# Kernel tuning notes

Hardware: AMD Instinct MI355X
Metric: run time of the kernel (lower is better)

Reference implementation:

```python
import jax, jax.numpy as jnp
import numpy as np

IMG_H, IMG_W = 256, 704  # full image shape (img_metas['img_shape'])
EPS = 1e-5
B, N_CAM, D_REF, C_CH = 1, 6, 1, 256
HF, WF = 32, 88
DD = 64
BEV_H = BEV_W = 128
Q = BEV_H * BEV_W


def inverse_sigmoid(x, eps=1e-5):
    x = jnp.clip(x, 0.0, 1.0)
    return jnp.log(jnp.clip(x, eps) / jnp.clip(1.0 - x, eps))


def grid_sample_2d(feat, grid):
    # feat [N,C,H,W], grid [N,Hg,Wg,2] (x,y in [-1,1]); bilinear, zeros padding, align_corners=False
    Nn, C, H, W = feat.shape
    x = (grid[..., 0] + 1.0) * 0.5 * W - 0.5
    y = (grid[..., 1] + 1.0) * 0.5 * H - 0.5
    x0 = jnp.floor(x)
    y0 = jnp.floor(y)
    wx = x - x0
    wy = y - y0
    x0 = x0.astype(jnp.int32)
    y0 = y0.astype(jnp.int32)

    def gather(ix, iy):
        valid = (ix >= 0) & (ix < W) & (iy >= 0) & (iy < H)
        ixc = jnp.clip(ix, 0, W - 1)
        iyc = jnp.clip(iy, 0, H - 1)
        v = jax.vmap(lambda f, jx, jy: f[:, jy, jx])(feat, ixc, iyc)  # [N,C,Hg,Wg]
        return v * valid[:, None].astype(feat.dtype)

    return (gather(x0, y0) * ((1 - wx) * (1 - wy))[:, None]
            + gather(x0 + 1, y0) * (wx * (1 - wy))[:, None]
            + gather(x0, y0 + 1) * ((1 - wx) * wy)[:, None]
            + gather(x0 + 1, y0 + 1) * (wx * wy)[:, None])


def grid_sample_3d(vol, grid):
    # vol [N,C,D,H,W], grid [N,Dg,Hg,Wg,3] (x,y,z); trilinear, zeros padding, align_corners=False
    Nn, C, D, H, W = vol.shape
    x = (grid[..., 0] + 1.0) * 0.5 * W - 0.5
    y = (grid[..., 1] + 1.0) * 0.5 * H - 0.5
    z = (grid[..., 2] + 1.0) * 0.5 * D - 0.5
    x0 = jnp.floor(x); y0 = jnp.floor(y); z0 = jnp.floor(z)
    wx = x - x0; wy = y - y0; wz = z - z0
    x0 = x0.astype(jnp.int32); y0 = y0.astype(jnp.int32); z0 = z0.astype(jnp.int32)

    def gather(ix, iy, iz):
        valid = (ix >= 0) & (ix < W) & (iy >= 0) & (iy < H) & (iz >= 0) & (iz < D)
        ixc = jnp.clip(ix, 0, W - 1)
        iyc = jnp.clip(iy, 0, H - 1)
        izc = jnp.clip(iz, 0, D - 1)
        v = jax.vmap(lambda f, jx, jy, jz: f[:, jz, jy, jx])(vol, ixc, iyc, izc)
        return v * valid[:, None].astype(vol.dtype)

    return (gather(x0, y0, z0) * ((1 - wx) * (1 - wy) * (1 - wz))[:, None]
            + gather(x0 + 1, y0, z0) * (wx * (1 - wy) * (1 - wz))[:, None]
            + gather(x0, y0 + 1, z0) * ((1 - wx) * wy * (1 - wz))[:, None]
            + gather(x0 + 1, y0 + 1, z0) * (wx * wy * (1 - wz))[:, None]
            + gather(x0, y0, z0 + 1) * ((1 - wx) * (1 - wy) * wz)[:, None]
            + gather(x0 + 1, y0, z0 + 1) * (wx * (1 - wy) * wz)[:, None]
            + gather(x0, y0 + 1, z0 + 1) * ((1 - wx) * wy * wz)[:, None]
            + gather(x0 + 1, y0 + 1, z0 + 1) * (wx * wy * wz)[:, None])


def setup_inputs() -> dict:
    key = jax.random.key(0)
    ks = jax.random.split(key, 12)
    feat = jax.random.normal(ks[0], (B * N_CAM, C_CH, HF, WF), jnp.float32)
    bev_queries = jax.random.normal(ks[1], (B, Q, C_CH), jnp.float32)
    bev_pos = jax.random.normal(ks[2], (B, Q, C_CH), jnp.float32)
    reference_points = jax.random.uniform(ks[3], (B, D_REF, Q, 3), jnp.float32)
    pc_range = jnp.array([-51.2, -51.2, -5.0, 51.2, 51.2, 3.0], jnp.float32)
    # semi-realistic lidar->image projection matrices: intrinsics * axis-swap * yaw per camera
    f, cx, cy = 500.0, IMG_W / 2.0, IMG_H / 2.0
    K = np.array([[f, 0, cx, 0], [0, f, cy, 0], [0, 0, 1, 0], [0, 0, 0, 1]], np.float32)
    A = np.array([[0, -1, 0, 0], [0, 0, -1, 0], [1, 0, 0, 0], [0, 0, 0, 1]], np.float32)
    mats = []
    for i in range(N_CAM):
        th = 2.0 * np.pi * i / N_CAM
        c, s = np.cos(th), np.sin(th)
        R = np.array([[c, s, 0, 0], [-s, c, 0, 0], [0, 0, 1, 0], [0, 0, 0, 1]], np.float32)
        mats.append(K @ A @ R)
    lidar_to_img = jnp.asarray(np.stack(mats))[None]  # [1,N,4,4]
    depth_prob = jax.random.uniform(ks[4], (B * N_CAM, DD, HF, WF), jnp.float32)
    sc = 0.02
    return {
        'feat': feat, 'bev_queries': bev_queries, 'bev_pos': bev_pos,
        'reference_points': reference_points, 'pc_range': pc_range,
        'lidar_to_img': lidar_to_img, 'depth_prob': depth_prob,
        'w_pos': jax.random.normal(ks[5], (C_CH, 1), jnp.float32) * sc,
        'b_pos': jnp.zeros((1,), jnp.float32),
        'w_img': jax.random.normal(ks[6], (C_CH, N_CAM * 2), jnp.float32) * sc,
        'b_img': jnp.zeros((N_CAM * 2,), jnp.float32),
        'w_att': jax.random.normal(ks[7], (C_CH, N_CAM), jnp.float32) * sc,
        'b_att': jnp.zeros((N_CAM,), jnp.float32),
        'conv_w': jax.random.normal(ks[8], (C_CH, C_CH, 3, 3), jnp.float32) * sc,
        'conv_b': jnp.zeros((C_CH,), jnp.float32),
        'bn_gamma': jnp.ones((C_CH,), jnp.float32),
        'bn_beta': jnp.zeros((C_CH,), jnp.float32),
        'bn_mean': jnp.zeros((C_CH,), jnp.float32),
        'bn_var': jnp.ones((C_CH,), jnp.float32),
        'se_w': jax.random.normal(ks[9], (C_CH, C_CH), jnp.float32) * sc,
        'se_b': jnp.zeros((C_CH,), jnp.float32),
        'cbam_w': jax.random.normal(ks[10], (1, 2, 7, 7), jnp.float32) * 0.05,
        'cbam_b': jnp.zeros((1,), jnp.float32),
        'bev_h': BEV_H, 'bev_w': BEV_W,
    }


def reference(feat, bev_queries, bev_pos, reference_points, pc_range, lidar_to_img, depth_prob,
              w_pos, b_pos, w_img, b_img, w_att, b_att, conv_w, conv_b,
              bn_gamma, bn_beta, bn_mean, bn_var, se_w, se_b, cbam_w, cbam_b, bev_h, bev_w):
    Bq, Qn = bev_queries.shape[:2]
    D = reference_points.shape[1]
    N = lidar_to_img.shape[1]
    BN, C, Hf, Wf = feat.shape
    q = bev_queries + bev_pos
    pos_offset = q @ w_pos + b_pos  # [B,Q,1] (only_use_height)
    z = jax.nn.sigmoid(inverse_sigmoid(reference_points[..., 2:3]) + pos_offset[:, None])
    rp = jnp.concatenate([reference_points[..., :2], z], axis=-1)  # [B,D,Q,3]
    attn = (q @ w_att + b_att).reshape(Bq, 1, Qn, N, 1)
    img_off = q @ w_img + b_img  # [B,Q,2N]
    # unnormalize to lidar coords; apply_3d_transformation == identity (no aug)
    pts = rp * (pc_range[3:] - pc_range[:3]) + pc_range[:3]
    pts4 = jnp.concatenate([pts, jnp.ones_like(pts[..., :1])], axis=-1)  # [B,D,Q,4]
    cam = jnp.einsum('bnij,bdqj->dbnqi', lidar_to_img, pts4)  # [D,B,N,Q,4]
    ref_depth = cam[..., 2:3]
    mask = ref_depth > EPS
    xy = cam[..., :2] / jnp.maximum(cam[..., 2:3], EPS)
    xy = xy / jnp.array([IMG_W, IMG_H], dtype=xy.dtype)
    xy = (xy - 0.5) * 2.0
    mask = mask & (xy[..., 0:1] > -1.0) & (xy[..., 0:1] < 1.0) & (xy[..., 1:2] > -1.0) & (xy[..., 1:2] < 1.0)
    Dd = depth_prob.shape[1]
    ref_depth = (ref_depth / Dd - 0.5) * 2.0
    mask = mask & (ref_depth > -1.0) & (ref_depth < 1.0)
    bev_mask = jnp.transpose(mask, (1, 4, 3, 2, 0)).astype(feat.dtype)  # [B,1,Q,N,D]
    off = img_off.reshape(Bq, Qn, N, 2).transpose(0, 2, 1, 3)[None] / jnp.array([Wf, Hf], dtype=feat.dtype)
    xy = xy + off  # [D,B,N,Q,2]
    grid = xy.transpose(1, 2, 3, 0, 4).reshape(BN, Qn, D, 2)
    sampled = grid_sample_2d(feat, grid).reshape(Bq, N, C, Qn, D).transpose(0, 2, 3, 1, 4)  # [B,C,Q,N,D]
    grid3 = jnp.concatenate([xy, ref_depth], axis=-1).transpose(1, 2, 3, 0, 4).reshape(BN, 1, Qn, D, 3)
    dp = grid_sample_3d(depth_prob[:, None], grid3).reshape(Bq, N, 1, Qn, D).transpose(0, 2, 3, 1, 4)
    bev_mask = jnp.nan_to_num(dp) * bev_mask
    w = jax.nn.sigmoid(attn) * jnp.nan_to_num(bev_mask)
    agg = (jnp.nan_to_num(sampled) * w)[..., 0].sum(-1)  # [B,C,Q] (D==1)
    x = agg.reshape(Bq, C, bev_h, bev_w)
    dn = ('NCHW', 'OIHW', 'NCHW')
    x = jax.lax.conv_general_dilated(x, conv_w, (1, 1), ((1, 1), (1, 1)), dimension_numbers=dn) + conv_b[None, :, None, None]
    x = (x - bn_mean[None, :, None, None]) * (bn_gamma / jnp.sqrt(bn_var + 1e-5))[None, :, None, None] + bn_beta[None, :, None, None]
    x = jax.nn.relu(x)
    s = x.mean(axis=(2, 3))  # SE: global avg pool + 1x1 conv + sigmoid
    x = x * jax.nn.sigmoid(s @ se_w.T + se_b)[:, :, None, None]
    a = jnp.concatenate([x.max(axis=1, keepdims=True), x.mean(axis=1, keepdims=True)], axis=1)  # CBAM spatial
    a = jax.lax.conv_general_dilated(a, cbam_w, (1, 1), ((3, 3), (3, 3)), dimension_numbers=dn) + cbam_b[None, :, None, None]
    x = x * jax.nn.sigmoid(a)
    out = x.reshape(Bq, C, bev_h * bev_w).transpose(0, 2, 1)
    return out, rp
```

## Files before the change

### kernel.cpp

```cpp
#include <hip/hip_runtime.h>
#include <math.h>

#define QN   16384
#define CCH  256
#define NCAM 6
#define HFD  32
#define WFD  88
#define DDD  64
#define BEVH 128
#define BEVW 128
#define IMGW 704.0f
#define IMGH 256.0f
#define EPSV 1e-5f

typedef __attribute__((ext_vector_type(8))) short bf8_t;
typedef __attribute__((ext_vector_type(8))) unsigned short us8;
typedef __attribute__((ext_vector_type(4))) unsigned short us4;
typedef __attribute__((ext_vector_type(4))) float f4_t;

__device__ __forceinline__ float sigmoidf_(float x){ return 1.0f/(1.0f+__expf(-x)); }

__device__ __forceinline__ unsigned short f2bf(float f){
    unsigned int b = __float_as_uint(f);
    b += 0x7FFFu + ((b >> 16) & 1u);
    return (unsigned short)(b >> 16);
}
__device__ __forceinline__ float bf2f(unsigned short u){
    return __uint_as_float(((unsigned int)u) << 16);
}

__global__ __launch_bounds__(256) void k_prep(const float* __restrict__ feat, unsigned short* __restrict__ feat_tH,
                                              const float* __restrict__ cw, unsigned short* __restrict__ wtH,
                                              float* __restrict__ ssum){
    int b = blockIdx.x;
    if (b < 4224){
        __shared__ float tile[32][33];
        int n   = b / 704;
        int rem = b - n*704;
        int cb  = (rem / 88) * 32;
        int pb  = (rem % 88) * 32;
        int tx = threadIdx.x & 31, ty = threadIdx.x >> 5;
        for (int r = ty; r < 32; r += 8)
            tile[r][tx] = feat[(size_t)(n*256 + cb + r)*2816 + pb + tx];
        __syncthreads();
        for (int r = ty; r < 32; r += 8)
            feat_tH[(size_t)(n*2816 + pb + r)*256 + cb + tx] = f2bf(tile[tx][r]);
    } else {
        int b2 = b - 4224;
        if (b2 == 0) ssum[threadIdx.x] = 0.f;
        int idx = b2*256 + threadIdx.x;
        int ci = idx & 255;
        int co = (idx >> 8) & 255;
        int kk = idx >> 16;
        wtH[idx] = f2bf(cw[(size_t)(co*256 + ci)*9 + kk]);
    }
}

__global__ __launch_bounds__(256) void k_geomagg(
    const float* __restrict__ bq, const float* __restrict__ bpos,
    const float* __restrict__ refp, const float* __restrict__ pcr,
    const float* __restrict__ l2i, const float* __restrict__ dpr,
    const float* __restrict__ w_pos, const float* __restrict__ b_pos,
    const float* __restrict__ w_img, const float* __restrict__ b_img,
    const float* __restrict__ w_att, const float* __restrict__ b_att,
    const unsigned short* __restrict__ feat_tH,
    unsigned short* __restrict__ aggH, float* __restrict__ out_rp)
{
    __shared__ float wl[19][256];
    __shared__ int   so_l[192];
    __shared__ float sw_l[192];
    int q0 = blockIdx.x * 8;
    int tid = threadIdx.x;
    int wid = tid >> 6, lane = tid & 63;
    int c0 = lane * 4;

    wl[0][tid] = w_pos[tid];
    #pragma unroll
    for (int r = 0; r < 6; r++){
        int idx = r*256 + tid;
        int c = idx / 6, j = idx - 6*c;
        wl[1 + j][c] = w_att[idx];
    }
    #pragma unroll
    for (int r = 0; r < 12; r++){
        int idx = r*256 + tid;
        int c = idx / 12, j = idx - 12*c;
        wl[7 + j][c] = w_img[idx];
    }
    __syncthreads();

    #pragma unroll
    for (int qi = 0; qi < 2; qi++){
        int ql = wid*2 + qi;
        int q  = q0 + ql;

        const float4 a4 = *(const float4*)(bq  + (size_t)q*CCH + c0);
        const float4 b4 = *(const float4*)(bpos+ (size_t)q*CCH + c0);
        float qv[4] = {a4.x+b4.x, a4.y+b4.y, a4.z+b4.z, a4.w+b4.w};

        float s[19];
        #pragma unroll
        for (int j = 0; j < 19; j++){
            const float4 wv = *(const float4*)&wl[j][c0];
            s[j] = qv[0]*wv.x + qv[1]*wv.y + qv[2]*wv.z + qv[3]*wv.w;
        }
        #pragma unroll
        for (int off=1; off<64; off<<=1){
            #pragma unroll
            for (int i=0;i<19;i++) s[i] += __shfl_xor(s[i], off, 64);
        }

        float pos_off = s[0] + b_pos[0];
        float rx = refp[q*3+0], ry = refp[q*3+1], rz = refp[q*3+2];
        float zc_ = fminf(fmaxf(rz, 0.f), 1.f);
        float inv = logf(fmaxf(zc_, EPSV) / fmaxf(1.f - zc_, EPSV));
        float znew = sigmoidf_(inv + pos_off);

        if (lane == 0){
            out_rp[q*3+0] = rx; out_rp[q*3+1] = ry; out_rp[q*3+2] = znew;
        }
        if (lane < NCAM){
            int n = lane;
            float att  = s[1+n] + b_att[n];
            float offx = (s[7+2*n]   + b_img[2*n])   / (float)WFD;
            float offy = (s[7+2*n+1] + b_img[2*n+1]) / (float)HFD;
            float lo0=pcr[0], lo1=pcr[1], lo2=pcr[2];
            float hi0=pcr[3], hi1=pcr[4], hi2=pcr[5];
            float px = rx*(hi0-lo0)+lo0, py = ry*(hi1-lo1)+lo1, pz = znew*(hi2-lo2)+lo2;
            const float* M = l2i + n*16;
            float cx = M[0]*px + M[1]*py + M[2]*pz  + M[3];
            float cy = M[4]*px + M[5]*py + M[6]*pz  + M[7];
            float cz = M[8]*px + M[9]*py + M[10]*pz + M[11];
            bool m = cz > EPSV;
            float zdiv = fmaxf(cz, EPSV);
            float u = (cx/zdiv)/IMGW; u = (u - 0.5f)*2.f;
            float v = (cy/zdiv)/IMGH; v = (v - 0.5f)*2.f;
            m = m && (u > -1.f) && (u < 1.f) && (v > -1.f) && (v < 1.f);
            float rdn = (cz/(float)DDD - 0.5f)*2.f;
            m = m && (rdn > -1.f) && (rdn < 1.f);

            int base = ql*24 + n*4;
            float wq = 0.f, xs = 0.f, ys = 0.f;
            if (m){
                float u2 = u + offx, v2 = v + offy;
                xs = (u2 + 1.f)*0.5f*WFD - 0.5f;
                ys = (v2 + 1.f)*0.5f*HFD - 0.5f;
                float zs = (rdn + 1.f)*0.5f*DDD - 0.5f;
                float fx = floorf(xs), fy = floorf(ys), fz = floorf(zs);
                int x0=(int)fx, y0=(int)fy, z0=(int)fz;
                float wx = xs-fx, wy = ys-fy, wz = zs-fz;
                float dp = 0.f;
                const float* vol = dpr + (size_t)n*DDD*HFD*WFD;
                #pragma unroll
                for (int dz=0; dz<2; dz++)
                #pragma unroll
                for (int dy=0; dy<2; dy++)
                #pragma unroll
                for (int dx=0; dx<2; dx++){
                    int ix=x0+dx, iy=y0+dy, iz=z0+dz;
                    if (ix>=0 && ix<WFD && iy>=0 && iy<HFD && iz>=0 && iz<DDD){
                        float ww = (dx?wx:1.f-wx)*(dy?wy:1.f-wy)*(dz?wz:1.f-wz);
                        dp += ww * vol[(size_t)(iz*HFD+iy)*WFD + ix];
                    }
                }
                wq = sigmoidf_(att) * dp;
            }
            if (m && wq != 0.f){
                float fx = floorf(xs), fy = floorf(ys);
                int x0=(int)fx, y0=(int)fy;
                float wx = xs-fx, wy = ys-fy;
                float cwv[4] = {(1.f-wx)*(1.f-wy), wx*(1.f-wy), (1.f-wx)*wy, wx*wy};
                int xi[4] = {x0, x0+1, x0, x0+1};
                int yi[4] = {y0, y0, y0+1, y0+1};
                #pragma unroll
                for (int k=0;k<4;k++){
                    bool ok = (xi[k]>=0 && xi[k]<WFD && yi[k]>=0 && yi[k]<HFD);
                    so_l[base+k] = ok ? ((n*HFD + yi[k])*WFD + xi[k]) : 0;
                    sw_l[base+k] = ok ? wq*cwv[k] : 0.f;
                }
            } else {
                #pragma unroll
                for (int k=0;k<4;k++){ so_l[base+k] = 0; sw_l[base+k] = 0.f; }
            }
        }
    }
    __syncthreads();

    int c4 = lane * 4;
    #pragma unroll
    for (int qi=0; qi<2; qi++){
        int ql = wid*2 + qi;
        float a0=0.f, a1=0.f, a2=0.f, a3=0.f;
        #pragma unroll
        for (int k=0;k<24;k++){
            float w = sw_l[ql*24+k];
            if (w != 0.f){
                us4 v = *(const us4*)(feat_tH + (size_t)so_l[ql*24+k]*CCH + c4);
                a0 += w * bf2f(v.x);
                a1 += w * bf2f(v.y);
                a2 += w * bf2f(v.z);
                a3 += w * bf2f(v.w);
            }
        }
        us4 o; o.x = f2bf(a0); o.y = f2bf(a1); o.z = f2bf(a2); o.w = f2bf(a3);
        *(us4*)(aggH + (size_t)(q0+ql)*CCH + c4) = o;
    }
}

__global__ __launch_bounds__(512, 4) void k_conv2(const unsigned short* __restrict__ aggH,
    const unsigned short* __restrict__ wtH, const float* __restrict__ conv_b,
    const float* __restrict__ bn_g, const float* __restrict__ bn_b,
    const float* __restrict__ bn_m, const float* __restrict__ bn_v,
    float* __restrict__ xN, float* __restrict__ ssum)
{
    __shared__ unsigned short Al[130][72];
    __shared__ unsigned short Bl[3][64][72];
    __shared__ float sacc[64];

    int h   = blockIdx.x;
    int co0 = blockIdx.y * 64;
    int tid  = threadIdx.x;
    int lane = tid & 63, wid = tid >> 6;
    int m_wave = (wid & 3) * 32;
    int n_wave = (wid >> 2) * 32;
    int l15 = lane & 15, quad = lane >> 4;

    f4_t acc[2][2];
    #pragma unroll
    for (int i=0;i<2;i++)
    #pragma unroll
    for (int j=0;j<2;j++) acc[i][j] = (f4_t){0.f,0.f,0.f,0.f};

    int aw = tid >> 2;
    int sa = (tid & 3) * 16;
    int bco = tid >> 3;
    int sb  = (tid & 7) * 8;

    if (tid < 8){
        int r = (tid >> 2) ? 129 : 0;
        int sg = (tid & 3) * 16;
        us8 z = (us8){0,0,0,0,0,0,0,0};
        *(us8*)&Al[r][sg]   = z;
        *(us8*)&Al[r][sg+8] = z;
    }
    if (tid < 64) sacc[tid] = 0.f;

    us8 ra0, ra1, rb0, rb1, rb2;
    const us8 z8 = (us8){0,0,0,0,0,0,0,0};

    #define LOADSTAGE(s) { \
        int kh_ = (s) >> 2; int ci0_ = ((s) & 3) << 6; \
        int ph_ = h + kh_ - 1; \
        if (ph_ >= 0 && ph_ < BEVH){ \
            const unsigned short* ap_ = aggH + ((size_t)(ph_*BEVW + aw)*CCH + ci0_ + sa); \
            ra0 = *(const us8*)ap_; ra1 = *(const us8*)(ap_ + 8); \
        } else { ra0 = z8; ra1 = z8; } \
        const unsigned short* bp_ = wtH + ((size_t)(kh_*3*256) + co0 + bco)*CCH + ci0_ + sb; \
        rb0 = *(const us8*)bp_; \
        rb1 = *(const us8*)(bp_ + 256*CCH); \
        rb2 = *(const us8*)(bp_ + 512*CCH); \
    }

    LOADSTAGE(0);
    for (int s=0; s<12; s++){
        __syncthreads();
        *(us8*)&Al[aw+1][sa]   = ra0;
        *(us8*)&Al[aw+1][sa+8] = ra1;
        *(us8*)&Bl[0][bco][sb] = rb0;
        *(us8*)&Bl[1][bco][sb] = rb1;
        *(us8*)&Bl[2][bco][sb] = rb2;
        __syncthreads();
        if (s < 11) LOADSTAGE(s+1);
        #pragma unroll
        for (int kw=0; kw<3; kw++){
            #pragma unroll
            for (int ks=0; ks<2; ks++){
                bf8_t af0 = *(bf8_t*)&Al[m_wave      + l15 + kw][ks*32 + quad*8];
                bf8_t af1 = *(bf8_t*)&Al[m_wave + 16 + l15 + kw][ks*32 + quad*8];
                bf8_t bf0 = *(bf8_t*)&Bl[kw][n_wave      + l15][ks*32 + quad*8];
                bf8_t bf1 = *(bf8_t*)&Bl[kw][n_wave + 16 + l15][ks*32 + quad*8];
                acc[0][0] = __builtin_amdgcn_mfma_f32_16x16x32_bf16(af0, bf0, acc[0][0], 0, 0, 0);
                acc[0][1] = __builtin_amdgcn_mfma_f32_16x16x32_bf16(af0, bf1, acc[0][1], 0, 0, 0);
                acc[1][0] = __builtin_amdgcn_mfma_f32_16x16x32_bf16(af1, bf0, acc[1][0], 0, 0, 0);
                acc[1][1] = __builtin_amdgcn_mfma_f32_16x16x32_bf16(af1, bf1, acc[1][1], 0, 0, 0);
            }
        }
    }
    #undef LOADSTAGE

    #pragma unroll
    for (int j=0;j<2;j++){
        int col = n_wave + j*16 + l15;
        int co = co0 + col;
        float sc = bn_g[co] * rsqrtf(bn_v[co] + 1e-5f);
        float sh = bn_b[co] - bn_m[co]*sc;
        float cb = conv_b[co];
        float part = 0.f;
        #pragma unroll
        for (int i=0;i<2;i++){
            #pragma unroll
            for (int r=0;r<4;r++){
                int m = m_wave + i*16 + quad*4 + r;
                int p = h*BEVW + m;
                float y = fmaxf((acc[i][j][r] + cb)*sc + sh, 0.f);
                xN[(size_t)p*CCH + co] = y;
                part += y;
            }
        }
        atomicAdd(&sacc[col], part);
    }
    __syncthreads();
    if (tid < 64) atomicAdd(&ssum[co0 + tid], sacc[tid]);
}

__global__ __launch_bounds__(256) void k_maps2(const float* __restrict__ xN,
    const float* __restrict__ ssum, const float* __restrict__ se_w, const float* __restrict__ se_b,
    float* __restrict__ scale_g, float* __restrict__ amax, float* __restrict__ amean)
{
    __shared__ float smv[256];
    __shared__ float scl[256];
    int t = threadIdx.x;
    smv[t] = ssum[t] * (1.f/16384.f);
    __syncthreads();
    float acc = se_b[t];
    for (int k=0; k<256; k+=4){
        float4 w4 = *(const float4*)&se_w[(size_t)t*256 + k];
        acc += smv[k]*w4.x + smv[k+1]*w4.y + smv[k+2]*w4.z + smv[k+3]*w4.w;
    }
    float sv = sigmoidf_(acc);
    scl[t] = sv;
    if (blockIdx.x == 0) scale_g[t] = sv;
    __syncthreads();

    int wid = t >> 6, lane = t & 63;
    int p0 = blockIdx.x * 64;
    float4 sc = *(const float4*)&scl[lane*4];
    for (int i=0; i<16; i++){
        int p = p0 + i*4 + wid;
        float4 v = *(const float4*)&xN[(size_t)p*CCH + lane*4];
        float a = v.x*sc.x, b = v.y*sc.y, c = v.z*sc.z, d = v.w*sc.w;
        float mx = fmaxf(fmaxf(a,b), fmaxf(c,d));
        float sm = a+b+c+d;
        #pragma unroll
        for (int off=1; off<64; off<<=1){
            mx = fmaxf(mx, __shfl_xor(mx, off, 64));
            sm += __shfl_xor(sm, off, 64);
        }
        if (lane == 0){ amax[p] = mx; amean[p] = sm*(1.f/256.f); }
    }
}

__global__ __launch_bounds__(256) void k_final2(const float* __restrict__ xN,
    const float* __restrict__ scale_g, const float* __restrict__ amax, const float* __restrict__ amean,
    const float* __restrict__ cw, const float* __restrict__ cb, float* __restrict__ out)
{
    __shared__ float am2[7][128];
    __shared__ float av2[7][128];
    __shared__ float wcb[98];
    __shared__ float scl[256];
    __shared__ float amap_l[64];

    int b = blockIdx.x;
    int h  = b >> 1;
    int w0 = (b & 1) * 64;
    int t = threadIdx.x;

    scl[t] = scale_g[t];
    if (t < 98) wcb[t] = cw[t];
    for (int idx = t; idx < 896; idx += 256){
        int r = idx >> 7, c = idx & 127;
        int ph = h + r - 3;
        bool ok = (ph >= 0 && ph < BEVH);
        am2[r][c] = ok ? amax[ph*BEVW + c] : 0.f;
        av2[r][c] = ok ? amean[ph*BEVW + c] : 0.f;
    }
    __syncthreads();

    if (t < 64){
        int px = w0 + t;
        float acc = cb[0];
        #pragma unroll
        for (int kh=0; kh<7; kh++){
            #pragma unroll
            for (int kw=0; kw<7; kw++){
                int pw = px + kw - 3;
                if (pw >= 0 && pw < BEVW)
                    acc += am2[kh][pw]*wcb[kh*7+kw] + av2[kh][pw]*wcb[49 + kh*7+kw];
            }
        }
        amap_l[t] = sigmoidf_(acc);
    }
    __syncthreads();

    int lane = t & 63, sub = t >> 6;
    int c4 = lane * 4;
    float4 sc = *(const float4*)&scl[c4];
    for (int i=0; i<16; i++){
        int pxl = sub*16 + i;
        int p = h*BEVW + w0 + pxl;
        float am = amap_l[pxl];
        float4 v = *(const float4*)&xN[(size_t)p*CCH + c4];
        float4 o;
        o.x = v.x*sc.x*am; o.y = v.y*sc.y*am; o.z = v.z*sc.z*am; o.w = v.w*sc.w*am;
        *(float4*)&out[(size_t)p*CCH + c4] = o;
    }
}

extern "C" void kernel_launch(void* const* d_in, const int* in_sizes, int n_in,
                              void* d_out, int out_size, void* d_ws, size_t ws_size,
                              hipStream_t stream) {
    const float* feat   = (const float*)d_in[0];
    const float* bq     = (const float*)d_in[1];
    const float* bpos   = (const float*)d_in[2];
    const float* refp   = (const float*)d_in[3];
    const float* pcr    = (const float*)d_in[4];
    const float* l2i    = (const float*)d_in[5];
    const float* dpr    = (const float*)d_in[6];
    const float* w_pos  = (const float*)d_in[7];
    const float* b_pos  = (const float*)d_in[8];
    const float* w_img  = (const float*)d_in[9];
    const float* b_img  = (const float*)d_in[10];
    const float* w_att  = (const float*)d_in[11];
    const float* b_att  = (const float*)d_in[12];
    const float* conv_w = (const float*)d_in[13];
    const float* conv_b = (const float*)d_in[14];
    const float* bn_g   = (const float*)d_in[15];
    const float* bn_b   = (const float*)d_in[16];
    const float* bn_m   = (const float*)d_in[17];
    const float* bn_v   = (const float*)d_in[18];
    const float* se_w   = (const float*)d_in[19];
    const float* se_b   = (const float*)d_in[20];
    const float* cbw    = (const float*)d_in[21];
    const float* cbb    = (const float*)d_in[22];
    float* out = (float*)d_out;

    float* ws = (float*)d_ws;
    size_t o = 0;
    unsigned short* feat_tH = (unsigned short*)(ws + o); o += (size_t)6*2816*128;
    unsigned short* wtH  = (unsigned short*)(ws + o); o += (size_t)9*256*128;
    unsigned short* aggH = (unsigned short*)(ws + o); o += (size_t)QN*128;
    float* xN      = ws + o;  o += (size_t)QN*256;
    float* ssum    = ws + o;  o += 256;
    float* scale_g = ws + o;  o += 256;
    float* amax    = ws + o;  o += QN;
    float* amean   = ws + o;  o += QN;

    k_prep<<<6528, 256, 0, stream>>>(feat, feat_tH, conv_w, wtH, ssum);
    k_geomagg<<<2048, 256, 0, stream>>>(bq, bpos, refp, pcr, l2i, dpr,
                                        w_pos, b_pos, w_img, b_img, w_att, b_att,
                                        feat_tH, aggH, out + (size_t)QN*256);
    k_conv2<<<dim3(128,4), 512, 0, stream>>>(aggH, wtH, conv_b, bn_g, bn_b, bn_m, bn_v, xN, ssum);
    k_maps2<<<256, 256, 0, stream>>>(xN, ssum, se_w, se_b, scale_g, amax, amean);
    k_final2<<<256, 256, 0, stream>>>(xN, scale_g, amax, amean, cbw, cbb, out);
}
```

Before: 246.1 us.

## Retile conv to 128x128 per block, relayout weights, transpose SE weights, widen gather

The 3x3 conv kernel moves from 512-thread blocks computing a 128x64 tile to 256-thread blocks computing a 128x128 tile with a 4x4 MFMA accumulator per wave. Conv weights are pre-laid out per stage so B-tile loads are contiguous. The geometry stage now spreads the six camera projections across two queries per wave through shared memory, and the gather uses 8-wide bf16 loads. The SE weights are transposed once in prep so the matvec reads coalesced columns. In exchange, conv blocks drop to 256 and register pressure rises, so occupancy may fall.

```diff
diff --git a/kernel.cpp b/kernel.cpp
--- a/kernel.cpp
+++ b/kernel.cpp
@@ -31,6 +31,7 @@
 
 __global__ __launch_bounds__(256) void k_prep(const float* __restrict__ feat, unsigned short* __restrict__ feat_tH,
                                               const float* __restrict__ cw, unsigned short* __restrict__ wtH,
+                                              const float* __restrict__ se_w, float* __restrict__ se_wT,
                                               float* __restrict__ ssum){
     int b = blockIdx.x;
     if (b < 4224){
@@ -45,14 +46,28 @@
         __syncthreads();
         for (int r = ty; r < 32; r += 8)
             feat_tH[(size_t)(n*2816 + pb + r)*256 + cb + tx] = f2bf(tile[tx][r]);
-    } else {
+    } else if (b < 6528){
         int b2 = b - 4224;
         if (b2 == 0) ssum[threadIdx.x] = 0.f;
         int idx = b2*256 + threadIdx.x;
         int ci = idx & 255;
         int co = (idx >> 8) & 255;
         int kk = idx >> 16;
-        wtH[idx] = f2bf(cw[(size_t)(co*256 + ci)*9 + kk]);
+        int kh = kk/3, kw = kk - kh*3;
+        int chunk = ci >> 6, ciin = ci & 63;
+        size_t dst = ((((size_t)(kh*4 + chunk)*3 + kw)*256 + co) << 6) + ciin;
+        wtH[dst] = f2bf(cw[(size_t)(co*256 + ci)*9 + kk]);
+    } else {
+        __shared__ float tile[32][33];
+        int tb = b - 6528;
+        int rb_ = (tb >> 3) * 32;
+        int cb_ = (tb & 7) * 32;
+        int tx = threadIdx.x & 31, ty = threadIdx.x >> 5;
+        for (int r = ty; r < 32; r += 8)
+            tile[r][tx] = se_w[(size_t)(rb_ + r)*256 + cb_ + tx];
+        __syncthreads();
+        for (int r = ty; r < 32; r += 8)
+            se_wT[(size_t)(cb_ + r)*256 + rb_ + tx] = tile[tx][r];
     }
 }
 
@@ -67,6 +82,7 @@
     unsigned short* __restrict__ aggH, float* __restrict__ out_rp)
 {
     __shared__ float wl[19][256];
+    __shared__ float sprj[8][24];
     __shared__ int   so_l[192];
     __shared__ float sw_l[192];
     int q0 = blockIdx.x * 8;
@@ -110,20 +126,29 @@
             for (int i=0;i<19;i++) s[i] += __shfl_xor(s[i], off, 64);
         }
 
-        float pos_off = s[0] + b_pos[0];
-        float rx = refp[q*3+0], ry = refp[q*3+1], rz = refp[q*3+2];
-        float zc_ = fminf(fmaxf(rz, 0.f), 1.f);
-        float inv = logf(fmaxf(zc_, EPSV) / fmaxf(1.f - zc_, EPSV));
-        float znew = sigmoidf_(inv + pos_off);
-
         if (lane == 0){
+            float pos_off = s[0] + b_pos[0];
+            float rx = refp[q*3+0], ry = refp[q*3+1], rz = refp[q*3+2];
+            float zc_ = fminf(fmaxf(rz, 0.f), 1.f);
+            float inv = logf(fmaxf(zc_, EPSV) / fmaxf(1.f - zc_, EPSV));
+            float znew = sigmoidf_(inv + pos_off);
             out_rp[q*3+0] = rx; out_rp[q*3+1] = ry; out_rp[q*3+2] = znew;
-        }
-        if (lane < NCAM){
-            int n = lane;
-            float att  = s[1+n] + b_att[n];
-            float offx = (s[7+2*n]   + b_img[2*n])   / (float)WFD;
-            float offy = (s[7+2*n+1] + b_img[2*n+1]) / (float)HFD;
+            #pragma unroll
+            for (int j=0;j<19;j++) sprj[ql][j] = s[j];
+            sprj[ql][19] = znew; sprj[ql][20] = rx; sprj[ql][21] = ry;
+        }
+    }
+    __syncthreads();
+
+    {
+        int sub = lane >> 5;
+        int n   = lane & 31;
+        if (n < NCAM){
+            int ql = wid*2 + sub;
+            float att  = sprj[ql][1+n] + b_att[n];
+            float offx = (sprj[ql][7+2*n] + b_img[2*n])   / (float)WFD;
+            float offy = (sprj[ql][8+2*n] + b_img[2*n+1]) / (float)HFD;
+            float znew = sprj[ql][19], rx = sprj[ql][20], ry = sprj[ql][21];
             float lo0=pcr[0], lo1=pcr[1], lo2=pcr[2];
             float hi0=pcr[3], hi1=pcr[4], hi2=pcr[5];
             float px = rx*(hi0-lo0)+lo0, py = ry*(hi1-lo1)+lo1, pz = znew*(hi2-lo2)+lo2;
@@ -186,121 +211,132 @@
     }
     __syncthreads();
 
-    int c4 = lane * 4;
-    #pragma unroll
-    for (int qi=0; qi<2; qi++){
-        int ql = wid*2 + qi;
-        float a0=0.f, a1=0.f, a2=0.f, a3=0.f;
+    {
+        int half = lane >> 5, li = lane & 31;
+        int c8 = li * 8;
+        int ql = wid*2 + half;
+        float a[8] = {0.f,0.f,0.f,0.f,0.f,0.f,0.f,0.f};
         #pragma unroll
         for (int k=0;k<24;k++){
             float w = sw_l[ql*24+k];
             if (w != 0.f){
-                us4 v = *(const us4*)(feat_tH + (size_t)so_l[ql*24+k]*CCH + c4);
-                a0 += w * bf2f(v.x);
-                a1 += w * bf2f(v.y);
-                a2 += w * bf2f(v.z);
-                a3 += w * bf2f(v.w);
-            }
-        }
-        us4 o; o.x = f2bf(a0); o.y = f2bf(a1); o.z = f2bf(a2); o.w = f2bf(a3);
-        *(us4*)(aggH + (size_t)(q0+ql)*CCH + c4) = o;
-    }
-}
-
-__global__ __launch_bounds__(512, 4) void k_conv2(const unsigned short* __restrict__ aggH,
+                us8 v = *(const us8*)(feat_tH + (size_t)so_l[ql*24+k]*CCH + c8);
+                #pragma unroll
+                for (int j=0;j<8;j++) a[j] += w * bf2f((unsigned short)v[j]);
+            }
+        }
+        us8 o;
+        #pragma unroll
+        for (int j=0;j<8;j++) o[j] = f2bf(a[j]);
+        *(us8*)(aggH + (size_t)(q0+ql)*CCH + c8) = o;
+    }
+}
+
+__global__ __launch_bounds__(256, 2) void k_conv2(const unsigned short* __restrict__ aggH,
     const unsigned short* __restrict__ wtH, const float* __restrict__ conv_b,
     const float* __restrict__ bn_g, const float* __restrict__ bn_b,
     const float* __restrict__ bn_m, const float* __restrict__ bn_v,
     float* __restrict__ xN, float* __restrict__ ssum)
 {
     __shared__ unsigned short Al[130][72];
-    __shared__ unsigned short Bl[3][64][72];
-    __shared__ float sacc[64];
+    __shared__ unsigned short Bl[3][128][72];
+    __shared__ float sacc[128];
 
     int h   = blockIdx.x;
-    int co0 = blockIdx.y * 64;
+    int co0 = blockIdx.y * 128;
     int tid  = threadIdx.x;
     int lane = tid & 63, wid = tid >> 6;
-    int m_wave = (wid & 3) * 32;
-    int n_wave = (wid >> 2) * 32;
+    int m_q = (wid & 1) * 64;
+    int n_q = (wid >> 1) * 64;
     int l15 = lane & 15, quad = lane >> 4;
 
-    f4_t acc[2][2];
-    #pragma unroll
-    for (int i=0;i<2;i++)
-    #pragma unroll
-    for (int j=0;j<2;j++) acc[i][j] = (f4_t){0.f,0.f,0.f,0.f};
-
-    int aw = tid >> 2;
-    int sa = (tid & 3) * 16;
-    int bco = tid >> 3;
-    int sb  = (tid & 7) * 8;
-
-    if (tid < 8){
-        int r = (tid >> 2) ? 129 : 0;
-        int sg = (tid & 3) * 16;
-        us8 z = (us8){0,0,0,0,0,0,0,0};
-        *(us8*)&Al[r][sg]   = z;
-        *(us8*)&Al[r][sg+8] = z;
-    }
-    if (tid < 64) sacc[tid] = 0.f;
-
-    us8 ra0, ra1, rb0, rb1, rb2;
+    f4_t acc[4][4];
+    #pragma unroll
+    for (int i=0;i<4;i++)
+    #pragma unroll
+    for (int j=0;j<4;j++) acc[i][j] = (f4_t){0.f,0.f,0.f,0.f};
+
+    int arow = tid >> 1;
+    int aseg = (tid & 1) * 32;
+
+    if (tid < 16){
+        int r = (tid >> 3) ? 129 : 0;
+        int sg = (tid & 7) * 8;
+        *(us8*)&Al[r][sg] = (us8){0,0,0,0,0,0,0,0};
+    }
+    if (tid < 128) sacc[tid] = 0.f;
+
+    us8 ra[4], rb[3][4];
     const us8 z8 = (us8){0,0,0,0,0,0,0,0};
 
     #define LOADSTAGE(s) { \
         int kh_ = (s) >> 2; int ci0_ = ((s) & 3) << 6; \
         int ph_ = h + kh_ - 1; \
         if (ph_ >= 0 && ph_ < BEVH){ \
-            const unsigned short* ap_ = aggH + ((size_t)(ph_*BEVW + aw)*CCH + ci0_ + sa); \
-            ra0 = *(const us8*)ap_; ra1 = *(const us8*)(ap_ + 8); \
-        } else { ra0 = z8; ra1 = z8; } \
-        const unsigned short* bp_ = wtH + ((size_t)(kh_*3*256) + co0 + bco)*CCH + ci0_ + sb; \
-        rb0 = *(const us8*)bp_; \
-        rb1 = *(const us8*)(bp_ + 256*CCH); \
-        rb2 = *(const us8*)(bp_ + 512*CCH); \
+            const unsigned short* ap_ = aggH + ((size_t)(ph_*BEVW + arow)*CCH + ci0_ + aseg); \
+            ra[0] = *(const us8*)ap_;      ra[1] = *(const us8*)(ap_ + 8); \
+            ra[2] = *(const us8*)(ap_ + 16); ra[3] = *(const us8*)(ap_ + 24); \
+        } else { ra[0]=z8; ra[1]=z8; ra[2]=z8; ra[3]=z8; } \
+        const unsigned short* bp_ = wtH + (size_t)(s)*49152 + (size_t)co0*64; \
+        _Pragma("unroll") \
+        for (int kw_=0; kw_<3; kw_++){ \
+            _Pragma("unroll") \
+            for (int j_=0; j_<4; j_++) \
+                rb[kw_][j_] = *(const us8*)(bp_ + kw_*16384 + (j_*256 + tid)*8); \
+        } \
     }
 
     LOADSTAGE(0);
     for (int s=0; s<12; s++){
         __syncthreads();
-        *(us8*)&Al[aw+1][sa]   = ra0;
-        *(us8*)&Al[aw+1][sa+8] = ra1;
-        *(us8*)&Bl[0][bco][sb] = rb0;
-        *(us8*)&Bl[1][bco][sb] = rb1;
-        *(us8*)&Bl[2][bco][sb] = rb2;
+        *(us8*)&Al[arow+1][aseg]      = ra[0];
+        *(us8*)&Al[arow+1][aseg+8]    = ra[1];
+        *(us8*)&Al[arow+1][aseg+16]   = ra[2];
+        *(us8*)&Al[arow+1][aseg+24]   = ra[3];
+        {
+            int bco = tid >> 3;
+            int ciin = (tid & 7) * 8;
+            #pragma unroll
+            for (int kw_=0; kw_<3; kw_++){
+                #pragma unroll
+                for (int j_=0; j_<4; j_++)
+                    *(us8*)&Bl[kw_][j_*32 + bco][ciin] = rb[kw_][j_];
+            }
+        }
         __syncthreads();
         if (s < 11) LOADSTAGE(s+1);
         #pragma unroll
-        for (int kw=0; kw<3; kw++){
-            #pragma unroll
-            for (int ks=0; ks<2; ks++){
-                bf8_t af0 = *(bf8_t*)&Al[m_wave      + l15 + kw][ks*32 + quad*8];
-                bf8_t af1 = *(bf8_t*)&Al[m_wave + 16 + l15 + kw][ks*32 + quad*8];
-                bf8_t bf0 = *(bf8_t*)&Bl[kw][n_wave      + l15][ks*32 + quad*8];
-                bf8_t bf1 = *(bf8_t*)&Bl[kw][n_wave + 16 + l15][ks*32 + quad*8];
-                acc[0][0] = __builtin_amdgcn_mfma_f32_16x16x32_bf16(af0, bf0, acc[0][0], 0, 0, 0);
-                acc[0][1] = __builtin_amdgcn_mfma_f32_16x16x32_bf16(af0, bf1, acc[0][1], 0, 0, 0);
-                acc[1][0] = __builtin_amdgcn_mfma_f32_16x16x32_bf16(af1, bf0, acc[1][0], 0, 0, 0);
-                acc[1][1] = __builtin_amdgcn_mfma_f32_16x16x32_bf16(af1, bf1, acc[1][1], 0, 0, 0);
+        for (int ks=0; ks<2; ks++){
+            #pragma unroll
+            for (int kw=0; kw<3; kw++){
+                bf8_t af[4], bfr[4];
+                #pragma unroll
+                for (int i=0;i<4;i++) af[i]  = *(bf8_t*)&Al[m_q + i*16 + l15 + kw][ks*32 + quad*8];
+                #pragma unroll
+                for (int j=0;j<4;j++) bfr[j] = *(bf8_t*)&Bl[kw][n_q + j*16 + l15][ks*32 + quad*8];
+                #pragma unroll
+                for (int i=0;i<4;i++)
+                #pragma unroll
+                for (int j=0;j<4;j++)
+                    acc[i][j] = __builtin_amdgcn_mfma_f32_16x16x32_bf16(af[i], bfr[j], acc[i][j], 0, 0, 0);
             }
         }
     }
     #undef LOADSTAGE
 
     #pragma unroll
-    for (int j=0;j<2;j++){
-        int col = n_wave + j*16 + l15;
+    for (int j=0;j<4;j++){
+        int col = n_q + j*16 + l15;
         int co = co0 + col;
         float sc = bn_g[co] * rsqrtf(bn_v[co] + 1e-5f);
         float sh = bn_b[co] - bn_m[co]*sc;
         float cb = conv_b[co];
         float part = 0.f;
         #pragma unroll
-        for (int i=0;i<2;i++){
+        for (int i=0;i<4;i++){
             #pragma unroll
             for (int r=0;r<4;r++){
-                int m = m_wave + i*16 + quad*4 + r;
+                int m = m_q + i*16 + quad*4 + r;
                 int p = h*BEVW + m;
                 float y = fmaxf((acc[i][j][r] + cb)*sc + sh, 0.f);
                 xN[(size_t)p*CCH + co] = y;
@@ -310,11 +346,11 @@
         atomicAdd(&sacc[col], part);
     }
     __syncthreads();
-    if (tid < 64) atomicAdd(&ssum[co0 + tid], sacc[tid]);
+    if (tid < 128) atomicAdd(&ssum[co0 + tid], sacc[tid]);
 }
 
 __global__ __launch_bounds__(256) void k_maps2(const float* __restrict__ xN,
-    const float* __restrict__ ssum, const float* __restrict__ se_w, const float* __restrict__ se_b,
+    const float* __restrict__ ssum, const float* __restrict__ se_wT, const float* __restrict__ se_b,
     float* __restrict__ scale_g, float* __restrict__ amax, float* __restrict__ amean)
 {
     __shared__ float smv[256];
@@ -322,12 +358,14 @@
     int t = threadIdx.x;
     smv[t] = ssum[t] * (1.f/16384.f);
     __syncthreads();
-    float acc = se_b[t];
+    float a0=0.f, a1=0.f, a2=0.f, a3=0.f;
     for (int k=0; k<256; k+=4){
-        float4 w4 = *(const float4*)&se_w[(size_t)t*256 + k];
-        acc += smv[k]*w4.x + smv[k+1]*w4.y + smv[k+2]*w4.z + smv[k+3]*w4.w;
-    }
-    float sv = sigmoidf_(acc);
+        a0 += smv[k]   * se_wT[(size_t)(k  )*256 + t];
+        a1 += smv[k+1] * se_wT[(size_t)(k+1)*256 + t];
+        a2 += smv[k+2] * se_wT[(size_t)(k+2)*256 + t];
+        a3 += smv[k+3] * se_wT[(size_t)(k+3)*256 + t];
+    }
+    float sv = sigmoidf_(se_b[t] + ((a0+a1)+(a2+a3)));
     scl[t] = sv;
     if (blockIdx.x == 0) scale_g[t] = sv;
     __syncthreads();
@@ -440,16 +478,17 @@
     unsigned short* wtH  = (unsigned short*)(ws + o); o += (size_t)9*256*128;
     unsigned short* aggH = (unsigned short*)(ws + o); o += (size_t)QN*128;
     float* xN      = ws + o;  o += (size_t)QN*256;
+    float* se_wT   = ws + o;  o += (size_t)256*256;
     float* ssum    = ws + o;  o += 256;
     float* scale_g = ws + o;  o += 256;
     float* amax    = ws + o;  o += QN;
     float* amean   = ws + o;  o += QN;
 
-    k_prep<<<6528, 256, 0, stream>>>(feat, feat_tH, conv_w, wtH, ssum);
+    k_prep<<<6592, 256, 0, stream>>>(feat, feat_tH, conv_w, wtH, se_w, se_wT, ssum);
     k_geomagg<<<2048, 256, 0, stream>>>(bq, bpos, refp, pcr, l2i, dpr,
                                         w_pos, b_pos, w_img, b_img, w_att, b_att,
                                         feat_tH, aggH, out + (size_t)QN*256);
-    k_conv2<<<dim3(128,4), 512, 0, stream>>>(aggH, wtH, conv_b, bn_g, bn_b, bn_m, bn_v, xN, ssum);
-    k_maps2<<<256, 256, 0, stream>>>(xN, ssum, se_w, se_b, scale_g, amax, amean);
+    k_conv2<<<dim3(128,2), 256, 0, stream>>>(aggH, wtH, conv_b, bn_g, bn_b, bn_m, bn_v, xN, ssum);
+    k_maps2<<<256, 256, 0, stream>>>(xN, ssum, se_wT, se_b, scale_g, amax, amean);
     k_final2<<<256, 256, 0, stream>>>(xN, scale_g, amax, amean, cbw, cbb, out);
 }
```

Measured after the change: 238.5 us. 1.03x faster.
